# Performance work log

Hardware: AMD Instinct MI355X
Metric: run time of the kernel (lower is better)

Reference implementation:

```python
import jax, jax.numpy as jnp
import numpy as np

DIM = 1024
NUM_HEADS = 16
HEAD_DIM = DIM // NUM_HEADS
SCALE = HEAD_DIM ** -0.5


def setup_inputs() -> dict:
    key = jax.random.key(0)
    ks = jax.random.split(key, 5)
    x = jax.random.normal(ks[0], (4, 1024, DIM), dtype=jnp.float32)
    w_qkv = jax.random.normal(ks[1], (DIM, 3 * DIM), dtype=jnp.float32) * (DIM ** -0.5)
    b_qkv = jnp.zeros((3 * DIM,), dtype=jnp.float32)
    w_proj = jax.random.normal(ks[2], (DIM, DIM), dtype=jnp.float32) * (DIM ** -0.5)
    b_proj = jnp.zeros((DIM,), dtype=jnp.float32)
    return {"x": x, "w_qkv": w_qkv, "b_qkv": b_qkv, "w_proj": w_proj, "b_proj": b_proj}


def reference(x, w_qkv, b_qkv, w_proj, b_proj):
    B, N, C = x.shape
    qkv = x @ w_qkv + b_qkv                                  # [B, N, 3C]
    qkv = qkv.reshape(B, N, 3, NUM_HEADS, HEAD_DIM)
    qkv = jnp.transpose(qkv, (2, 0, 3, 1, 4))                # [3, B, H, N, d]
    q, k, v = qkv[0] * SCALE, qkv[1], qkv[2]
    # attn scores in float32 (clamp to finfo range is a no-op after the cast)
    attn = jnp.einsum('bhnd,bhmd->bhnm', q, k).astype(jnp.float32)
    f32 = jnp.finfo(jnp.float32)
    attn = jnp.clip(attn, f32.min, f32.max)
    attn = jax.nn.softmax(attn, axis=-1)
    out = jnp.einsum('bhnm,bhmd->bhnd', attn, v)             # [B, H, N, d]
    out = jnp.transpose(out, (0, 2, 1, 3)).reshape(B, N, C)
    return out @ w_proj + b_proj
```

## Files before the change

### kernel.cpp

```cpp
#include <hip/hip_runtime.h>


typedef _Float16 half8 __attribute__((ext_vector_type(8)));
typedef _Float16 half4v __attribute__((ext_vector_type(4)));
typedef float floatx4 __attribute__((ext_vector_type(4)));

#define MFMA16(a, b, c) __builtin_amdgcn_mfma_f32_16x16x32_f16((a), (b), (c), 0, 0, 0)

static constexpr int DIM = 1024;
static constexpr int BATCH = 4;
static constexpr int SEQ = 1024;
static constexpr int NH = 16;
static constexpr int HD = 64;
static constexpr float SCALE = 0.125f;

__device__ static inline void gld16(_Float16* lds, const _Float16* g) {
    __builtin_amdgcn_global_load_lds(
        (const __attribute__((address_space(1))) void*)g,
        (__attribute__((address_space(3))) void*)lds, 16, 0, 0);
}

__global__ __launch_bounds__(256) void convert_f32_f16(const float* __restrict__ in,
                                                       _Float16* __restrict__ out, int n) {
    int i = (blockIdx.x * 256 + threadIdx.x) * 4;
    if (i >= n) return;
    float4 v = *reinterpret_cast<const float4*>(in + i);
    half4v h;
    h.x = (_Float16)v.x; h.y = (_Float16)v.y; h.z = (_Float16)v.z; h.w = (_Float16)v.w;
    *reinterpret_cast<half4v*>(out + i) = h;
}

__global__ __launch_bounds__(256) void transpose_f32_f16(const float* __restrict__ in,
                                                         _Float16* __restrict__ out,
                                                         int R, int C) {
    __shared__ float tile[32][33];
    int c0 = blockIdx.x * 32, r0 = blockIdx.y * 32;
    int tx = threadIdx.x, ty = threadIdx.y;
#pragma unroll
    for (int j = 0; j < 32; j += 8)
        tile[ty + j][tx] = in[(r0 + ty + j) * C + (c0 + tx)];
    __syncthreads();
#pragma unroll
    for (int j = 0; j < 32; j += 8)
        out[(c0 + ty + j) * R + (r0 + tx)] = (_Float16)tile[tx][ty + j];
}

template <int MODE>
__global__ __launch_bounds__(256) void gemm_bt(const _Float16* __restrict__ A,
                                               const _Float16* __restrict__ Bt,
                                               const float* __restrict__ bias, int N,
                                               float* __restrict__ outF,
                                               _Float16* __restrict__ qbuf,
                                               _Float16* __restrict__ kbuf,
                                               _Float16* __restrict__ vtbuf) {
    constexpr int K = 1024;
    constexpr int BK = 32;
    __shared__ _Float16 Ah[128 * BK];
    __shared__ _Float16 Bh[128 * BK];

    const int tid = threadIdx.x;
    const int wid = tid >> 6;
    const int lane = tid & 63;
    const int g = lane >> 4;
    const int ln = lane & 15;
    const int wr = wid >> 1, wc = wid & 1;
    const int m0 = blockIdx.y * 128;
    const int n0 = blockIdx.x * 128;

    floatx4 acc[4][4];
#pragma unroll
    for (int i = 0; i < 4; ++i)
#pragma unroll
        for (int j = 0; j < 4; ++j) acc[i][j] = (floatx4){0.f, 0.f, 0.f, 0.f};

    const int lrow = lane >> 2;
    const int lk = (lane & 3) * 8;
    const _Float16* ga0 = A + (size_t)(m0 + wid * 16 + lrow) * K + lk;
    const _Float16* gb0 = Bt + (size_t)(n0 + wid * 16 + lrow) * K + lk;

    for (int kt = 0; kt < K / BK; ++kt) {
        const int k0 = kt * BK;
        __syncthreads();
        gld16(&Ah[(wid * 16) * BK], ga0 + k0);
        gld16(&Ah[(64 + wid * 16) * BK], ga0 + (size_t)64 * K + k0);
        gld16(&Bh[(wid * 16) * BK], gb0 + k0);
        gld16(&Bh[(64 + wid * 16) * BK], gb0 + (size_t)64 * K + k0);
        __syncthreads();

        half8 af[4], bf[4];
#pragma unroll
        for (int i = 0; i < 4; ++i)
            af[i] = *reinterpret_cast<const half8*>(&Ah[(wr * 64 + i * 16 + ln) * BK + g * 8]);
#pragma unroll
        for (int j = 0; j < 4; ++j)
            bf[j] = *reinterpret_cast<const half8*>(&Bh[(wc * 64 + j * 16 + ln) * BK + g * 8]);
#pragma unroll
        for (int i = 0; i < 4; ++i)
#pragma unroll
            for (int j = 0; j < 4; ++j) acc[i][j] = MFMA16(af[i], bf[j], acc[i][j]);
    }

#pragma unroll
    for (int i = 0; i < 4; ++i) {
#pragma unroll
        for (int j = 0; j < 4; ++j) {
            const int n = n0 + wc * 64 + j * 16 + ln;
            const float bn = bias[n];
            const int mrow = m0 + wr * 64 + i * 16 + g * 4;
            if (MODE == 0) {
                const int which = n >> 10;
                const int rem = n & 1023;
                const int h = rem >> 6;
                const int dd = rem & 63;
                const int b = mrow >> 10, tok = mrow & 1023;
                const int bh = b * NH + h;
                if (which == 2) {
                    half4v pk;
#pragma unroll
                    for (int r = 0; r < 4; ++r) pk[r] = (_Float16)(acc[i][j][r] + bn);
                    *reinterpret_cast<half4v*>(
                        &vtbuf[(size_t)((bh * HD + dd) << 10) + tok]) = pk;
                } else {
                    _Float16* dst = (which == 0) ? qbuf : kbuf;
                    const float sc = (which == 0) ? SCALE : 1.0f;
#pragma unroll
                    for (int r = 0; r < 4; ++r)
                        dst[(size_t)((bh << 10) + tok + r) * HD + dd] =
                            (_Float16)((acc[i][j][r] + bn) * sc);
                }
            } else {
#pragma unroll
                for (int r = 0; r < 4; ++r)
                    outF[(size_t)(mrow + r) * N + n] = acc[i][j][r] + bn;
            }
        }
    }
}

__global__ __launch_bounds__(256, 2) void flash_attn(const _Float16* __restrict__ qbuf,
                                                     const _Float16* __restrict__ kbuf,
                                                     const _Float16* __restrict__ vtbuf,
                                                     _Float16* __restrict__ attn_out) {
    __shared__ _Float16 Klds[2 * 2 * 64 * 32];
    __shared__ _Float16 Vlds[2 * 2 * 64 * 32];
    __shared__ _Float16 Plds[8 * 16 * 68];

    const int tid = threadIdx.x;
    const int wid = tid >> 6;
    const int lane = tid & 63;
    const int g = lane >> 4;
    const int ln = lane & 15;
    const int bh = blockIdx.x;
    const int qbase = blockIdx.y * 128 + wid * 32;
    const _Float16* qg = qbuf + ((size_t)bh << 10) * HD;
    const _Float16* kg = kbuf + ((size_t)bh << 10) * HD;
    const _Float16* vg = vtbuf + (size_t)bh * (HD * SEQ);

    const int srow = lane >> 2;
    const int sch = (lane & 3) * 8;

    half8 qf[2][2];
#pragma unroll
    for (int rg = 0; rg < 2; ++rg)
#pragma unroll
        for (int f = 0; f < 2; ++f)
            qf[rg][f] = *reinterpret_cast<const half8*>(
                qg + (size_t)(qbase + rg * 16 + ln) * HD + f * 32 + g * 8);

    floatx4 o[2][4];
#pragma unroll
    for (int rg = 0; rg < 2; ++rg)
#pragma unroll
        for (int t = 0; t < 4; ++t) o[rg][t] = (floatx4){0.f, 0.f, 0.f, 0.f};
    float l_lane[2][4] = {{0.f, 0.f, 0.f, 0.f}, {0.f, 0.f, 0.f, 0.f}};

    _Float16* Pw = Plds + (wid * 2) * 16 * 68;

#pragma unroll
    for (int f = 0; f < 2; ++f) {
        gld16(Klds + f * 2048 + (wid * 16) * 32,
              kg + (size_t)(wid * 16 + srow) * HD + f * 32 + sch);
        gld16(Vlds + f * 2048 + (wid * 16) * 32,
              vg + (size_t)(wid * 16 + srow) * SEQ + f * 32 + sch);
    }

    for (int kt = 0; kt < SEQ / 64; ++kt) {
        asm volatile("s_waitcnt vmcnt(0)" ::: "memory");
        asm volatile("s_barrier" ::: "memory");
        const int cur = kt & 1;
        if (kt < SEQ / 64 - 1) {
            const int kr1 = (kt + 1) * 64;
            _Float16* kb = Klds + (cur ^ 1) * 4096;
            _Float16* vb = Vlds + (cur ^ 1) * 4096;
#pragma unroll
            for (int f = 0; f < 2; ++f) {
                gld16(kb + f * 2048 + (wid * 16) * 32,
                      kg + (size_t)(kr1 + wid * 16 + srow) * HD + f * 32 + sch);
                gld16(vb + f * 2048 + (wid * 16) * 32,
                      vg + (size_t)(wid * 16 + srow) * SEQ + kr1 + f * 32 + sch);
            }
        }
        const _Float16* Kb = Klds + cur * 4096;
        const _Float16* Vb = Vlds + cur * 4096;

        half8 kf[4][2], vf[4][2];
#pragma unroll
        for (int c = 0; c < 4; ++c)
#pragma unroll
            for (int f = 0; f < 2; ++f) {
                kf[c][f] = *reinterpret_cast<const half8*>(
                    &Kb[f * 2048 + (c * 16 + ln) * 32 + g * 8]);
                vf[c][f] = *reinterpret_cast<const half8*>(
                    &Vb[f * 2048 + (c * 16 + ln) * 32 + g * 8]);
            }

        floatx4 s[2][4];
#pragma unroll
        for (int rg = 0; rg < 2; ++rg)
#pragma unroll
            for (int c = 0; c < 4; ++c) {
                floatx4 z = (floatx4){0.f, 0.f, 0.f, 0.f};
                z = MFMA16(qf[rg][0], kf[c][0], z);
                z = MFMA16(qf[rg][1], kf[c][1], z);
                s[rg][c] = z;
            }

#pragma unroll
        for (int rg = 0; rg < 2; ++rg)
#pragma unroll
            for (int c = 0; c < 4; ++c)
#pragma unroll
                for (int r = 0; r < 4; ++r) {
                    float p = __expf(s[rg][c][r]);
                    l_lane[rg][r] += p;
                    Pw[(rg * 16 + g * 4 + r) * 68 + c * 16 + ln] = (_Float16)p;
                }

        asm volatile("s_waitcnt lgkmcnt(0)" ::: "memory");

#pragma unroll
        for (int rg = 0; rg < 2; ++rg) {
            half8 pf0 = *reinterpret_cast<const half8*>(&Pw[(rg * 16 + ln) * 68 + g * 8]);
            half8 pf1 = *reinterpret_cast<const half8*>(&Pw[(rg * 16 + ln) * 68 + 32 + g * 8]);
#pragma unroll
            for (int t = 0; t < 4; ++t) {
                o[rg][t] = MFMA16(pf0, vf[t][0], o[rg][t]);
                o[rg][t] = MFMA16(pf1, vf[t][1], o[rg][t]);
            }
        }
    }

    const int b = bh >> 4, h = bh & 15;
#pragma unroll
    for (int rg = 0; rg < 2; ++rg)
#pragma unroll
        for (int r = 0; r < 4; ++r) {
            float l = l_lane[rg][r];
            l += __shfl_xor(l, 1);
            l += __shfl_xor(l, 2);
            l += __shfl_xor(l, 4);
            l += __shfl_xor(l, 8);
            const float inv = 1.0f / l;
            const int tok = qbase + rg * 16 + g * 4 + r;
            _Float16* dst = attn_out + (size_t)(b * SEQ + tok) * DIM + h * HD;
#pragma unroll
            for (int t = 0; t < 4; ++t) dst[t * 16 + ln] = (_Float16)(o[rg][t][r] * inv);
        }
}

extern "C" void kernel_launch(void* const* d_in, const int* in_sizes, int n_in,
                              void* d_out, int out_size, void* d_ws, size_t ws_size,
                              hipStream_t stream) {
    const float* x = (const float*)d_in[0];
    const float* wqkv = (const float*)d_in[1];
    const float* bqkv = (const float*)d_in[2];
    const float* wproj = (const float*)d_in[3];
    const float* bproj = (const float*)d_in[4];
    float* out = (float*)d_out;

    char* ws = (char*)d_ws;
    _Float16* xh     = (_Float16*)(ws);
    _Float16* wqkvT  = (_Float16*)(ws + (8ull << 20));
    _Float16* qbuf   = (_Float16*)(ws + (14ull << 20));
    _Float16* kbuf   = (_Float16*)(ws + (22ull << 20));
    _Float16* vtbuf  = (_Float16*)(ws + (30ull << 20));
    _Float16* attn   = xh;
    _Float16* wprojT = wqkvT;

    convert_f32_f16<<<4096, 256, 0, stream>>>(x, xh, BATCH * SEQ * DIM);
    transpose_f32_f16<<<dim3(96, 32), dim3(32, 8), 0, stream>>>(wqkv, wqkvT, DIM, 3 * DIM);
    gemm_bt<0><<<dim3(24, 32), 256, 0, stream>>>(xh, wqkvT, bqkv, 3 * DIM, nullptr,
                                                 qbuf, kbuf, vtbuf);
    transpose_f32_f16<<<dim3(32, 32), dim3(32, 8), 0, stream>>>(wproj, wprojT, DIM, DIM);
    flash_attn<<<dim3(BATCH * NH, SEQ / 128), 256, 0, stream>>>(qbuf, kbuf, vtbuf, attn);
    gemm_bt<1><<<dim3(8, 32), 256, 0, stream>>>(attn, wprojT, bproj, DIM, out,
                                                nullptr, nullptr, nullptr);
}
```

Before: 190.1 us.

## Fuse prep kernels and double-buffer GEMM LDS loads

Merges the x conversion and both weight transposes into a single prep launch, giving wprojT its own workspace region so it can be produced up front. The GEMM now double-buffers its LDS tiles, prefetching the next K slice while computing the current one, with one barrier per iteration instead of two, and sets launch_bounds to 2 blocks per CU. This aims to cut launch overhead and hide global-load latency, at the cost of twice the LDS per block and more workspace.

```diff
diff --git a/kernel.cpp b/kernel.cpp
--- a/kernel.cpp
+++ b/kernel.cpp
@@ -20,43 +20,59 @@
         (__attribute__((address_space(3))) void*)lds, 16, 0, 0);
 }
 
-__global__ __launch_bounds__(256) void convert_f32_f16(const float* __restrict__ in,
-                                                       _Float16* __restrict__ out, int n) {
-    int i = (blockIdx.x * 256 + threadIdx.x) * 4;
-    if (i >= n) return;
-    float4 v = *reinterpret_cast<const float4*>(in + i);
-    half4v h;
-    h.x = (_Float16)v.x; h.y = (_Float16)v.y; h.z = (_Float16)v.z; h.w = (_Float16)v.w;
-    *reinterpret_cast<half4v*>(out + i) = h;
-}
-
-__global__ __launch_bounds__(256) void transpose_f32_f16(const float* __restrict__ in,
-                                                         _Float16* __restrict__ out,
-                                                         int R, int C) {
+__global__ __launch_bounds__(256) void prep(const float* __restrict__ x,
+                                            _Float16* __restrict__ xh,
+                                            const float* __restrict__ wqkv,
+                                            _Float16* __restrict__ wqkvT,
+                                            const float* __restrict__ wproj,
+                                            _Float16* __restrict__ wprojT) {
     __shared__ float tile[32][33];
-    int c0 = blockIdx.x * 32, r0 = blockIdx.y * 32;
-    int tx = threadIdx.x, ty = threadIdx.y;
+    const int bid = blockIdx.x;
+    const int tid = threadIdx.x;
+    if (bid < 4096) {
+        int i = (bid * 256 + tid) * 4;
+        float4 v = *reinterpret_cast<const float4*>(x + i);
+        half4v h;
+        h[0] = (_Float16)v.x; h[1] = (_Float16)v.y;
+        h[2] = (_Float16)v.z; h[3] = (_Float16)v.w;
+        *reinterpret_cast<half4v*>(xh + i) = h;
+        return;
+    }
+    const float* in;
+    _Float16* out;
+    int R, C, bx, by;
+    if (bid < 7168) {
+        int b = bid - 4096;
+        in = wqkv; out = wqkvT; R = 1024; C = 3072;
+        bx = b % 96; by = b / 96;
+    } else {
+        int b = bid - 7168;
+        in = wproj; out = wprojT; R = 1024; C = 1024;
+        bx = b & 31; by = b >> 5;
+    }
+    const int c0 = bx * 32, r0 = by * 32;
+    const int tx = tid & 31, ty = tid >> 5;
 #pragma unroll
     for (int j = 0; j < 32; j += 8)
-        tile[ty + j][tx] = in[(r0 + ty + j) * C + (c0 + tx)];
+        tile[ty + j][tx] = in[(size_t)(r0 + ty + j) * C + (c0 + tx)];
     __syncthreads();
 #pragma unroll
     for (int j = 0; j < 32; j += 8)
-        out[(c0 + ty + j) * R + (r0 + tx)] = (_Float16)tile[tx][ty + j];
+        out[(size_t)(c0 + ty + j) * R + (r0 + tx)] = (_Float16)tile[tx][ty + j];
 }
 
 template <int MODE>
-__global__ __launch_bounds__(256) void gemm_bt(const _Float16* __restrict__ A,
-                                               const _Float16* __restrict__ Bt,
-                                               const float* __restrict__ bias, int N,
-                                               float* __restrict__ outF,
-                                               _Float16* __restrict__ qbuf,
-                                               _Float16* __restrict__ kbuf,
-                                               _Float16* __restrict__ vtbuf) {
+__global__ __launch_bounds__(256, 2) void gemm_bt(const _Float16* __restrict__ A,
+                                                  const _Float16* __restrict__ Bt,
+                                                  const float* __restrict__ bias, int N,
+                                                  float* __restrict__ outF,
+                                                  _Float16* __restrict__ qbuf,
+                                                  _Float16* __restrict__ kbuf,
+                                                  _Float16* __restrict__ vtbuf) {
     constexpr int K = 1024;
     constexpr int BK = 32;
-    __shared__ _Float16 Ah[128 * BK];
-    __shared__ _Float16 Bh[128 * BK];
+    __shared__ _Float16 Ah[2][128 * BK];
+    __shared__ _Float16 Bh[2][128 * BK];
 
     const int tid = threadIdx.x;
     const int wid = tid >> 6;
@@ -78,22 +94,32 @@
     const _Float16* ga0 = A + (size_t)(m0 + wid * 16 + lrow) * K + lk;
     const _Float16* gb0 = Bt + (size_t)(n0 + wid * 16 + lrow) * K + lk;
 
+    gld16(&Ah[0][(wid * 16) * BK], ga0);
+    gld16(&Ah[0][(64 + wid * 16) * BK], ga0 + (size_t)64 * K);
+    gld16(&Bh[0][(wid * 16) * BK], gb0);
+    gld16(&Bh[0][(64 + wid * 16) * BK], gb0 + (size_t)64 * K);
+
     for (int kt = 0; kt < K / BK; ++kt) {
-        const int k0 = kt * BK;
-        __syncthreads();
-        gld16(&Ah[(wid * 16) * BK], ga0 + k0);
-        gld16(&Ah[(64 + wid * 16) * BK], ga0 + (size_t)64 * K + k0);
-        gld16(&Bh[(wid * 16) * BK], gb0 + k0);
-        gld16(&Bh[(64 + wid * 16) * BK], gb0 + (size_t)64 * K + k0);
-        __syncthreads();
+        const int cur = kt & 1;
+        asm volatile("s_waitcnt vmcnt(0)" ::: "memory");
+        asm volatile("s_barrier" ::: "memory");
+        if (kt < K / BK - 1) {
+            const int k0 = (kt + 1) * BK;
+            gld16(&Ah[cur ^ 1][(wid * 16) * BK], ga0 + k0);
+            gld16(&Ah[cur ^ 1][(64 + wid * 16) * BK], ga0 + (size_t)64 * K + k0);
+            gld16(&Bh[cur ^ 1][(wid * 16) * BK], gb0 + k0);
+            gld16(&Bh[cur ^ 1][(64 + wid * 16) * BK], gb0 + (size_t)64 * K + k0);
+        }
 
         half8 af[4], bf[4];
 #pragma unroll
         for (int i = 0; i < 4; ++i)
-            af[i] = *reinterpret_cast<const half8*>(&Ah[(wr * 64 + i * 16 + ln) * BK + g * 8]);
+            af[i] = *reinterpret_cast<const half8*>(
+                &Ah[cur][(wr * 64 + i * 16 + ln) * BK + g * 8]);
 #pragma unroll
         for (int j = 0; j < 4; ++j)
-            bf[j] = *reinterpret_cast<const half8*>(&Bh[(wc * 64 + j * 16 + ln) * BK + g * 8]);
+            bf[j] = *reinterpret_cast<const half8*>(
+                &Bh[cur][(wc * 64 + j * 16 + ln) * BK + g * 8]);
 #pragma unroll
         for (int i = 0; i < 4; ++i)
 #pragma unroll
@@ -284,14 +310,12 @@
     _Float16* qbuf   = (_Float16*)(ws + (14ull << 20));
     _Float16* kbuf   = (_Float16*)(ws + (22ull << 20));
     _Float16* vtbuf  = (_Float16*)(ws + (30ull << 20));
+    _Float16* wprojT = (_Float16*)(ws + (38ull << 20));
     _Float16* attn   = xh;
-    _Float16* wprojT = wqkvT;
-
-    convert_f32_f16<<<4096, 256, 0, stream>>>(x, xh, BATCH * SEQ * DIM);
-    transpose_f32_f16<<<dim3(96, 32), dim3(32, 8), 0, stream>>>(wqkv, wqkvT, DIM, 3 * DIM);
+
+    prep<<<8192, 256, 0, stream>>>(x, xh, wqkv, wqkvT, wproj, wprojT);
     gemm_bt<0><<<dim3(24, 32), 256, 0, stream>>>(xh, wqkvT, bqkv, 3 * DIM, nullptr,
                                                  qbuf, kbuf, vtbuf);
-    transpose_f32_f16<<<dim3(32, 32), dim3(32, 8), 0, stream>>>(wproj, wprojT, DIM, DIM);
     flash_attn<<<dim3(BATCH * NH, SEQ / 128), 256, 0, stream>>>(qbuf, kbuf, vtbuf, attn);
     gemm_bt<1><<<dim3(8, 32), 256, 0, stream>>>(attn, wprojT, bproj, DIM, out,
                                                 nullptr, nullptr, nullptr);
```

After: 184.1 us. 3.2% less time.
